# Kernel optimization log

Hardware: AMD Instinct MI355X
Metric: run time of the kernel (lower is better)

## Reference

```python
import jax, jax.numpy as jnp
import numpy as np

K = 3          # kernel_size
STRIDE = 1
ITERS = 3      # num_iterations


def squash(t, axis=-1):
    sn = jnp.sum(t * t, axis=axis, keepdims=True)
    return (sn / (1.0 + sn)) * t / jnp.sqrt(sn)


def setup_inputs() -> dict:
    key = jax.random.key(0)
    k1, k2 = jax.random.split(key)
    B, Nin, H, Cin = 8, 32, 14, 8
    C, Cout = 32, 16
    R = Nin * K * K  # 288 route nodes
    x = jax.random.normal(k1, (B, Nin, H, H, Cin), dtype=jnp.float32)
    route_weights = jax.random.normal(k2, (C, R, Cin, Cout), dtype=jnp.float32)
    return {"x": x, "route_weights": route_weights}


def reference(x, route_weights):
    B, Nin, H, _, Cin = x.shape
    C, R, _, Cout = route_weights.shape
    w = (H - K) // STRIDE + 1

    # Extract all w*w spatial windows at once (instead of the python loop).
    rows = STRIDE * jnp.arange(w)[:, None] + jnp.arange(K)  # [w, K]
    win = x[:, :, rows]            # [B, Nin, w, K, W, Cin]
    win = win[:, :, :, :, rows]    # [B, Nin, w, K, w, K, Cin]
    # route-node order matches .view: (Nin, k, k) flattened
    win = win.transpose(0, 2, 4, 1, 3, 5, 6).reshape(B, w, w, R, Cin)

    priors = jnp.einsum('bpqri,crio->cbpqro', win, route_weights)

    # Dynamic routing (fixed small iteration count -> python loop is fine).
    logits = jnp.zeros_like(priors)
    out = None
    for i in range(ITERS):
        probs = jax.nn.softmax(logits, axis=4)  # softmax over route nodes (dim=2 in torch 5D layout)
        out = squash(jnp.sum(probs * priors, axis=4, keepdims=True))  # [C,B,w,w,1,Cout]
        if i != ITERS - 1:
            logits = logits + jnp.sum(priors * out, axis=-1, keepdims=True)

    out = out[:, :, :, :, 0, :]          # [C, B, w, w, Cout]
    return out.transpose(1, 0, 2, 3, 4)  # [B, C, w, w, Cout]
```

## Files before the change

### kernel.cpp

```cpp
#include <hip/hip_runtime.h>
#include <math.h>

namespace {
constexpr int NIN   = 32;
constexpr int H_    = 14;
constexpr int CIN   = 8;
constexpr int C_    = 32;
constexpr int COUT  = 16;
constexpr int R_    = 288;
constexpr int W_    = 12;
constexpr int NITER = 3;
constexpr int CH    = 32;
constexpr int NCH   = 9;
constexpr size_t XSUB = (size_t)NIN * H_ * H_ * CIN;
}

typedef unsigned int u32;
typedef const __attribute__((address_space(1))) u32* as1_u32p;
typedef __attribute__((address_space(3))) u32* as3_u32p;

__device__ __forceinline__ void async_copy16(const void* g, void* l) {
    __builtin_amdgcn_global_load_lds((as1_u32p)g, (as3_u32p)l, 16, 0, 0);
}
__device__ __forceinline__ float dot4(const float4 a, const float4 b) {
    return fmaf(a.x, b.x, fmaf(a.y, b.y, fmaf(a.z, b.z, a.w * b.w)));
}
__device__ __forceinline__ float dpp_add_xor1(float v) {
    int t = __builtin_amdgcn_update_dpp(0, __float_as_int(v), 0xB1, 0xF, 0xF, true);
    return v + __int_as_float(t);
}
__device__ __forceinline__ float dpp_add_xor2(float v) {
    int t = __builtin_amdgcn_update_dpp(0, __float_as_int(v), 0x4E, 0xF, 0xF, true);
    return v + __int_as_float(t);
}
__device__ __forceinline__ float dpp_add_shr4(float v) {
    int t = __builtin_amdgcn_update_dpp(0, __float_as_int(v), 0x114, 0xF, 0xF, true);
    return v + __int_as_float(t);
}
__device__ __forceinline__ float dpp_add_shr8(float v) {
    int t = __builtin_amdgcn_update_dpp(0, __float_as_int(v), 0x118, 0xF, 0xF, true);
    return v + __int_as_float(t);
}
template <int CTRL>
__device__ __forceinline__ float dpp_bc(float v) {
    return __int_as_float(
        __builtin_amdgcn_update_dpp(0, __float_as_int(v), CTRL, 0xF, 0xF, true));
}

__global__ __launch_bounds__(256)
void caps_routeC(const float* __restrict__ x,
                 const float* __restrict__ rw,
                 float* __restrict__ out)
{
    const int tid = threadIdx.x;
    const int p  = blockIdx.x / W_;
    const int q  = blockIdx.x % W_;
    const int b0 = blockIdx.y * 4;
    const int c  = blockIdx.z;

    __shared__ float4 wbuf[2][1024];
    __shared__ float  sRed[4][2][16];
    __shared__ float  redE[4][2];
    __shared__ float  vS[4][16];

    const int og   = tid & 3;
    const int rl   = tid >> 2;
    const int cr   = rl & 31;
    const int sh   = rl >> 5;
    const int lane = tid & 63;
    const int wv   = tid >> 6;
    const int sA   = sh * 2;

    const float* xq = x + (size_t)(b0 + sA + (og >> 1)) * XSUB + (og & 1) * 4;
    const float4* rwcF4 = (const float4*)(rw + (size_t)c * R_ * CIN * COUT);

    float4 xv;
    auto xld = [&](int k) {
        const int r  = k * CH + cr;
        const int n  = r / 9, rem = r - n * 9;
        const int kh = rem / 3, kw = rem - kh * 3;
        xv = *(const float4*)(xq + ((n * H_ + (p + kh)) * H_ + (q + kw)) * CIN);
    };

    auto stage = [&](int k, int buf) {
        const float4* gchunk = rwcF4 + (size_t)k * (CH * 32);
        #pragma unroll
        for (int t = 0; t < 4; ++t) {
            const int s   = t * 256 + tid;
            const int ii  = s >> 7;
            const int wcr = (s >> 2) & 31;
            async_copy16(gchunk + (wcr * 32 + ii * 4 + (s & 3)),
                         (char*)&wbuf[buf][0] + (t * 256 + (tid & 192)) * 16);
        }
    };

    float4 acc[NCH][2];

    xld(0);
    stage(0, 0);
    #pragma unroll
    for (int k = 0; k < NCH; ++k) {
        __syncthreads();
        if (k + 1 < NCH) stage(k + 1, (k + 1) & 1);
        const float4* wb = &wbuf[k & 1][0];
        const float4 cur = xv;
        float fA[8], fB[8];
        fA[0] = dpp_bc<0x00>(cur.x); fA[1] = dpp_bc<0x00>(cur.y);
        fA[2] = dpp_bc<0x00>(cur.z); fA[3] = dpp_bc<0x00>(cur.w);
        fA[4] = dpp_bc<0x55>(cur.x); fA[5] = dpp_bc<0x55>(cur.y);
        fA[6] = dpp_bc<0x55>(cur.z); fA[7] = dpp_bc<0x55>(cur.w);
        fB[0] = dpp_bc<0xAA>(cur.x); fB[1] = dpp_bc<0xAA>(cur.y);
        fB[2] = dpp_bc<0xAA>(cur.z); fB[3] = dpp_bc<0xAA>(cur.w);
        fB[4] = dpp_bc<0xFF>(cur.x); fB[5] = dpp_bc<0xFF>(cur.y);
        fB[6] = dpp_bc<0xFF>(cur.z); fB[7] = dpp_bc<0xFF>(cur.w);
        if (k + 1 < NCH) xld(k + 1);
        float4 a0 = make_float4(0.f, 0.f, 0.f, 0.f);
        float4 a1 = make_float4(0.f, 0.f, 0.f, 0.f);
        #pragma unroll
        for (int i = 0; i < 8; ++i) {
            const float4 wv4 = wb[i * 128 + cr * 4 + og];
            a0.x = fmaf(fA[i], wv4.x, a0.x);  a1.x = fmaf(fB[i], wv4.x, a1.x);
            a0.y = fmaf(fA[i], wv4.y, a0.y);  a1.y = fmaf(fB[i], wv4.y, a1.y);
            a0.z = fmaf(fA[i], wv4.z, a0.z);  a1.z = fmaf(fB[i], wv4.z, a1.z);
            a0.w = fmaf(fA[i], wv4.w, a0.w);  a1.w = fmaf(fB[i], wv4.w, a1.w);
        }
        acc[k][0] = a0;  acc[k][1] = a1;
    }

    float lgA[NCH], lgB[NCH];
    #pragma unroll
    for (int j = 0; j < NCH; ++j) { lgA[j] = 0.f; lgB[j] = 0.f; }

    for (int it = 0; it < NITER; ++it) {
        float4 s0 = make_float4(0.f, 0.f, 0.f, 0.f);
        float4 s1 = make_float4(0.f, 0.f, 0.f, 0.f);
        float se0 = 0.f, se1 = 0.f;

        if (it == 0) {
            #pragma unroll
            for (int j = 0; j < NCH; ++j) {
                s0.x += acc[j][0].x;  s1.x += acc[j][1].x;
                s0.y += acc[j][0].y;  s1.y += acc[j][1].y;
                s0.z += acc[j][0].z;  s1.z += acc[j][1].z;
                s0.w += acc[j][0].w;  s1.w += acc[j][1].w;
            }
        } else {
            const float4 v0 = *(const float4*)&vS[sA][og * 4];
            const float4 v1 = *(const float4*)&vS[sA + 1][og * 4];
            #pragma unroll
            for (int j = 0; j < NCH; ++j) {
                float d0 = dot4(acc[j][0], v0);
                float d1 = dot4(acc[j][1], v1);
                d0 = dpp_add_xor1(d0);  d1 = dpp_add_xor1(d1);
                d0 = dpp_add_xor2(d0);  d1 = dpp_add_xor2(d1);
                lgA[j] += d0;                 lgB[j] += d1;
                const float e0 = __expf(lgA[j]);
                const float e1 = __expf(lgB[j]);
                se0 += e0;                    se1 += e1;
                s0.x = fmaf(e0, acc[j][0].x, s0.x);  s1.x = fmaf(e1, acc[j][1].x, s1.x);
                s0.y = fmaf(e0, acc[j][0].y, s0.y);  s1.y = fmaf(e1, acc[j][1].y, s1.y);
                s0.z = fmaf(e0, acc[j][0].z, s0.z);  s1.z = fmaf(e1, acc[j][1].z, s1.z);
                s0.w = fmaf(e0, acc[j][0].w, s0.w);  s1.w = fmaf(e1, acc[j][1].w, s1.w);
            }
            se0 = dpp_add_shr4(se0);  se1 = dpp_add_shr4(se1);
            se0 = dpp_add_shr8(se0);  se1 = dpp_add_shr8(se1);
            se0 += __shfl_xor(se0, 16, 64);  se1 += __shfl_xor(se1, 16, 64);
            se0 += __shfl_xor(se0, 32, 64);  se1 += __shfl_xor(se1, 32, 64);
            if (lane == 15) { redE[wv][0] = se0; redE[wv][1] = se1; }
        }

        s0.x = dpp_add_shr4(s0.x);  s1.x = dpp_add_shr4(s1.x);
        s0.y = dpp_add_shr4(s0.y);  s1.y = dpp_add_shr4(s1.y);
        s0.z = dpp_add_shr4(s0.z);  s1.z = dpp_add_shr4(s1.z);
        s0.w = dpp_add_shr4(s0.w);  s1.w = dpp_add_shr4(s1.w);
        s0.x = dpp_add_shr8(s0.x);  s1.x = dpp_add_shr8(s1.x);
        s0.y = dpp_add_shr8(s0.y);  s1.y = dpp_add_shr8(s1.y);
        s0.z = dpp_add_shr8(s0.z);  s1.z = dpp_add_shr8(s1.z);
        s0.w = dpp_add_shr8(s0.w);  s1.w = dpp_add_shr8(s1.w);
        #pragma unroll
        for (int off = 16; off <= 32; off <<= 1) {
            s0.x += __shfl_xor(s0.x, off, 64);  s1.x += __shfl_xor(s1.x, off, 64);
            s0.y += __shfl_xor(s0.y, off, 64);  s1.y += __shfl_xor(s1.y, off, 64);
            s0.z += __shfl_xor(s0.z, off, 64);  s1.z += __shfl_xor(s1.z, off, 64);
            s0.w += __shfl_xor(s0.w, off, 64);  s1.w += __shfl_xor(s1.w, off, 64);
        }
        if (lane >= 12 && lane < 16) {
            *(float4*)&sRed[wv][0][(lane & 3) * 4] = s0;
            *(float4*)&sRed[wv][1][(lane & 3) * 4] = s1;
        }
        __syncthreads();

        if (tid < 64) {
            const int sub = tid >> 4;
            const int o   = tid & 15;
            const int g   = sub >> 1;
            const int l   = sub & 1;
            const float inv = (it == 0)
                ? (1.0f / (float)R_)
                : 1.0f / (redE[g * 2][l] + redE[g * 2 + 1][l]);
            float s = (sRed[g * 2][l][o] + sRed[g * 2 + 1][l][o]) * inv;
            float sn = s * s;
            sn = dpp_add_xor1(sn);
            sn = dpp_add_xor2(sn);
            sn += __shfl_xor(sn, 4, 64);
            sn += __shfl_xor(sn, 8, 64);
            const float v = s * (sqrtf(sn) / (1.0f + sn));
            if (it == NITER - 1) {
                out[((((size_t)(b0 + sub) * C_ + c) * W_ + p) * W_ + q) * COUT + o] = v;
            } else {
                vS[sub][o] = v;
            }
        }
        if (it == NITER - 1) break;
        __syncthreads();
    }
}

extern "C" void kernel_launch(void* const* d_in, const int* in_sizes, int n_in,
                              void* d_out, int out_size, void* d_ws, size_t ws_size,
                              hipStream_t stream) {
    const float* x  = (const float*)d_in[0];
    const float* rw = (const float*)d_in[1];
    float* out = (float*)d_out;
    dim3 grid(W_ * W_, 2, C_);
    caps_routeC<<<grid, 256, 0, stream>>>(x, rw, out);
}
```

Baseline: 188.3 us.

## Split weight staging between LDS and registers; redundantly compute squash per thread

Half of each weight chunk (input channels 4-7) is now loaded straight from global memory into registers and prefetched one chunk ahead, while only the other half goes through the async LDS double buffer, halving the LDS staging footprint. The routing-iteration epilogue no longer funnels through a single wave writing vS. Every thread reads the double-buffered partial sums, computes the squash itself, and keeps v in registers, which removes one __syncthreads per iteration. The cost is more redundant global loads per thread and duplicated squash math, plus higher register pressure.

```diff
diff --git a/kernel.cpp b/kernel.cpp
--- a/kernel.cpp
+++ b/kernel.cpp
@@ -48,20 +48,19 @@
 }
 
 __global__ __launch_bounds__(256)
-void caps_routeC(const float* __restrict__ x,
+void caps_routeE(const float* __restrict__ x,
                  const float* __restrict__ rw,
                  float* __restrict__ out)
 {
+    __shared__ __align__(16) float4 wbuf[2][512];
+    __shared__ __align__(16) float  sRed[2][4][2][16];
+    __shared__ float  redE[2][4][2];
+
     const int tid = threadIdx.x;
     const int p  = blockIdx.x / W_;
     const int q  = blockIdx.x % W_;
     const int b0 = blockIdx.y * 4;
     const int c  = blockIdx.z;
-
-    __shared__ float4 wbuf[2][1024];
-    __shared__ float  sRed[4][2][16];
-    __shared__ float  redE[4][2];
-    __shared__ float  vS[4][16];
 
     const int og   = tid & 3;
     const int rl   = tid >> 2;
@@ -73,6 +72,7 @@
 
     const float* xq = x + (size_t)(b0 + sA + (og >> 1)) * XSUB + (og & 1) * 4;
     const float4* rwcF4 = (const float4*)(rw + (size_t)c * R_ * CIN * COUT);
+    const float4* wgbase = rwcF4 + cr * 32 + og;
 
     float4 xv;
     auto xld = [&](int k) {
@@ -82,10 +82,16 @@
         xv = *(const float4*)(xq + ((n * H_ + (p + kh)) * H_ + (q + kw)) * CIN);
     };
 
+    float4 gw0, gw1, gw2, gw3;
+    auto wld = [&](int k) {
+        const float4* g = wgbase + (size_t)k * 1024;
+        gw0 = g[16]; gw1 = g[20]; gw2 = g[24]; gw3 = g[28];
+    };
+
     auto stage = [&](int k, int buf) {
         const float4* gchunk = rwcF4 + (size_t)k * (CH * 32);
         #pragma unroll
-        for (int t = 0; t < 4; ++t) {
+        for (int t = 0; t < 2; ++t) {
             const int s   = t * 256 + tid;
             const int ii  = s >> 7;
             const int wcr = (s >> 2) & 31;
@@ -96,8 +102,7 @@
 
     float4 acc[NCH][2];
 
-    xld(0);
-    stage(0, 0);
+    xld(0); wld(0); stage(0, 0);
     #pragma unroll
     for (int k = 0; k < NCH; ++k) {
         __syncthreads();
@@ -114,10 +119,31 @@
         fB[4] = dpp_bc<0xFF>(cur.x); fB[5] = dpp_bc<0xFF>(cur.y);
         fB[6] = dpp_bc<0xFF>(cur.z); fB[7] = dpp_bc<0xFF>(cur.w);
         if (k + 1 < NCH) xld(k + 1);
+
         float4 a0 = make_float4(0.f, 0.f, 0.f, 0.f);
         float4 a1 = make_float4(0.f, 0.f, 0.f, 0.f);
+        {
+            const float4 g0 = gw0, g1 = gw1, g2 = gw2, g3 = gw3;
+            if (k + 1 < NCH) wld(k + 1);
+            a0.x = fmaf(fA[4], g0.x, a0.x);  a1.x = fmaf(fB[4], g0.x, a1.x);
+            a0.y = fmaf(fA[4], g0.y, a0.y);  a1.y = fmaf(fB[4], g0.y, a1.y);
+            a0.z = fmaf(fA[4], g0.z, a0.z);  a1.z = fmaf(fB[4], g0.z, a1.z);
+            a0.w = fmaf(fA[4], g0.w, a0.w);  a1.w = fmaf(fB[4], g0.w, a1.w);
+            a0.x = fmaf(fA[5], g1.x, a0.x);  a1.x = fmaf(fB[5], g1.x, a1.x);
+            a0.y = fmaf(fA[5], g1.y, a0.y);  a1.y = fmaf(fB[5], g1.y, a1.y);
+            a0.z = fmaf(fA[5], g1.z, a0.z);  a1.z = fmaf(fB[5], g1.z, a1.z);
+            a0.w = fmaf(fA[5], g1.w, a0.w);  a1.w = fmaf(fB[5], g1.w, a1.w);
+            a0.x = fmaf(fA[6], g2.x, a0.x);  a1.x = fmaf(fB[6], g2.x, a1.x);
+            a0.y = fmaf(fA[6], g2.y, a0.y);  a1.y = fmaf(fB[6], g2.y, a1.y);
+            a0.z = fmaf(fA[6], g2.z, a0.z);  a1.z = fmaf(fB[6], g2.z, a1.z);
+            a0.w = fmaf(fA[6], g2.w, a0.w);  a1.w = fmaf(fB[6], g2.w, a1.w);
+            a0.x = fmaf(fA[7], g3.x, a0.x);  a1.x = fmaf(fB[7], g3.x, a1.x);
+            a0.y = fmaf(fA[7], g3.y, a0.y);  a1.y = fmaf(fB[7], g3.y, a1.y);
+            a0.z = fmaf(fA[7], g3.z, a0.z);  a1.z = fmaf(fB[7], g3.z, a1.z);
+            a0.w = fmaf(fA[7], g3.w, a0.w);  a1.w = fmaf(fB[7], g3.w, a1.w);
+        }
         #pragma unroll
-        for (int i = 0; i < 8; ++i) {
+        for (int i = 0; i < 4; ++i) {
             const float4 wv4 = wb[i * 128 + cr * 4 + og];
             a0.x = fmaf(fA[i], wv4.x, a0.x);  a1.x = fmaf(fB[i], wv4.x, a1.x);
             a0.y = fmaf(fA[i], wv4.y, a0.y);  a1.y = fmaf(fB[i], wv4.y, a1.y);
@@ -130,6 +156,8 @@
     float lgA[NCH], lgB[NCH];
     #pragma unroll
     for (int j = 0; j < NCH; ++j) { lgA[j] = 0.f; lgB[j] = 0.f; }
+
+    float4 v0, v1;
 
     for (int it = 0; it < NITER; ++it) {
         float4 s0 = make_float4(0.f, 0.f, 0.f, 0.f);
@@ -145,8 +173,6 @@
                 s0.w += acc[j][0].w;  s1.w += acc[j][1].w;
             }
         } else {
-            const float4 v0 = *(const float4*)&vS[sA][og * 4];
-            const float4 v1 = *(const float4*)&vS[sA + 1][og * 4];
             #pragma unroll
             for (int j = 0; j < NCH; ++j) {
                 float d0 = dot4(acc[j][0], v0);
@@ -166,7 +192,6 @@
             se0 = dpp_add_shr8(se0);  se1 = dpp_add_shr8(se1);
             se0 += __shfl_xor(se0, 16, 64);  se1 += __shfl_xor(se1, 16, 64);
             se0 += __shfl_xor(se0, 32, 64);  se1 += __shfl_xor(se1, 32, 64);
-            if (lane == 15) { redE[wv][0] = se0; redE[wv][1] = se1; }
         }
 
         s0.x = dpp_add_shr4(s0.x);  s1.x = dpp_add_shr4(s1.x);
@@ -184,35 +209,49 @@
             s0.z += __shfl_xor(s0.z, off, 64);  s1.z += __shfl_xor(s1.z, off, 64);
             s0.w += __shfl_xor(s0.w, off, 64);  s1.w += __shfl_xor(s1.w, off, 64);
         }
+        const int ib = it & 1;
         if (lane >= 12 && lane < 16) {
-            *(float4*)&sRed[wv][0][(lane & 3) * 4] = s0;
-            *(float4*)&sRed[wv][1][(lane & 3) * 4] = s1;
-        }
+            *(float4*)&sRed[ib][wv][0][(lane & 3) * 4] = s0;
+            *(float4*)&sRed[ib][wv][1][(lane & 3) * 4] = s1;
+        }
+        if (it && lane == 15) { redE[ib][wv][0] = se0; redE[ib][wv][1] = se1; }
         __syncthreads();
 
-        if (tid < 64) {
-            const int sub = tid >> 4;
-            const int o   = tid & 15;
-            const int g   = sub >> 1;
-            const int l   = sub & 1;
-            const float inv = (it == 0)
-                ? (1.0f / (float)R_)
-                : 1.0f / (redE[g * 2][l] + redE[g * 2 + 1][l]);
-            float s = (sRed[g * 2][l][o] + sRed[g * 2 + 1][l][o]) * inv;
-            float sn = s * s;
-            sn = dpp_add_xor1(sn);
-            sn = dpp_add_xor2(sn);
-            sn += __shfl_xor(sn, 4, 64);
-            sn += __shfl_xor(sn, 8, 64);
-            const float v = s * (sqrtf(sn) / (1.0f + sn));
-            if (it == NITER - 1) {
-                out[((((size_t)(b0 + sub) * C_ + c) * W_ + p) * W_ + q) * COUT + o] = v;
-            } else {
-                vS[sub][o] = v;
+        const float4 pA0 = *(const float4*)&sRed[ib][sA][0][og * 4];
+        const float4 pB0 = *(const float4*)&sRed[ib][sA + 1][0][og * 4];
+        const float4 pA1 = *(const float4*)&sRed[ib][sA][1][og * 4];
+        const float4 pB1 = *(const float4*)&sRed[ib][sA + 1][1][og * 4];
+        float inv0, inv1;
+        if (it == 0) {
+            inv0 = inv1 = 1.0f / (float)R_;
+        } else {
+            inv0 = 1.0f / (redE[ib][sA][0] + redE[ib][sA + 1][0]);
+            inv1 = 1.0f / (redE[ib][sA][1] + redE[ib][sA + 1][1]);
+        }
+        float4 ss0, ss1;
+        ss0.x = (pA0.x + pB0.x) * inv0;  ss1.x = (pA1.x + pB1.x) * inv1;
+        ss0.y = (pA0.y + pB0.y) * inv0;  ss1.y = (pA1.y + pB1.y) * inv1;
+        ss0.z = (pA0.z + pB0.z) * inv0;  ss1.z = (pA1.z + pB1.z) * inv1;
+        ss0.w = (pA0.w + pB0.w) * inv0;  ss1.w = (pA1.w + pB1.w) * inv1;
+        float sn0 = dot4(ss0, ss0);
+        float sn1 = dot4(ss1, ss1);
+        sn0 = dpp_add_xor1(sn0);  sn1 = dpp_add_xor1(sn1);
+        sn0 = dpp_add_xor2(sn0);  sn1 = dpp_add_xor2(sn1);
+        const float c0 = sqrtf(sn0) / (1.0f + sn0);
+        const float c1 = sqrtf(sn1) / (1.0f + sn1);
+        v0.x = ss0.x * c0;  v1.x = ss1.x * c1;
+        v0.y = ss0.y * c0;  v1.y = ss1.y * c1;
+        v0.z = ss0.z * c0;  v1.z = ss1.z * c1;
+        v0.w = ss0.w * c0;  v1.w = ss1.w * c1;
+
+        if (it == NITER - 1) {
+            if (cr < 2) {
+                const float4 vv = cr ? v1 : v0;
+                *(float4*)&out[((((size_t)(b0 + sA + cr) * C_ + c) * W_ + p) * W_ + q)
+                               * COUT + og * 4] = vv;
             }
-        }
-        if (it == NITER - 1) break;
-        __syncthreads();
+            break;
+        }
     }
 }
 
@@ -223,5 +262,5 @@
     const float* rw = (const float*)d_in[1];
     float* out = (float*)d_out;
     dim3 grid(W_ * W_, 2, C_);
-    caps_routeC<<<grid, 256, 0, stream>>>(x, rw, out);
-}
+    caps_routeE<<<grid, 256, 0, stream>>>(x, rw, out);
+}
```

Measured after the change: 194.1 us. +3.0%, slower.

## Make routing kernel persistent with cross-tile prefetch of weights and inputs

Applied to the files above, without the earlier changes.

Replaces the 9216-block grid with 1024 persistent blocks that each process 9 tiles. While the last chunk of the current tile is being computed, the block issues the async LDS copy of the next tile's first weight chunk and its first x load. The aim is to cut block launch and prologue cost and to hide each tile's initial load latency. The cost is a fixed grid that may leave some CUs unevenly loaded, plus extra registers for the next tile's state.

```diff
diff --git a/kernel.cpp b/kernel.cpp
--- a/kernel.cpp
+++ b/kernel.cpp
@@ -12,6 +12,8 @@
 constexpr int NITER = 3;
 constexpr int CH    = 32;
 constexpr int NCH   = 9;
+constexpr int NTILE = 9;
+constexpr int NBLK  = 1024;
 constexpr size_t XSUB = (size_t)NIN * H_ * H_ * CIN;
 }
 
@@ -48,21 +50,16 @@
 }
 
 __global__ __launch_bounds__(256)
-void caps_routeC(const float* __restrict__ x,
+void caps_routeF(const float* __restrict__ x,
                  const float* __restrict__ rw,
                  float* __restrict__ out)
 {
-    const int tid = threadIdx.x;
-    const int p  = blockIdx.x / W_;
-    const int q  = blockIdx.x % W_;
-    const int b0 = blockIdx.y * 4;
-    const int c  = blockIdx.z;
-
     __shared__ float4 wbuf[2][1024];
     __shared__ float  sRed[4][2][16];
     __shared__ float  redE[4][2];
     __shared__ float  vS[4][16];
 
+    const int tid = threadIdx.x;
     const int og   = tid & 3;
     const int rl   = tid >> 2;
     const int cr   = rl & 31;
@@ -71,19 +68,31 @@
     const int wv   = tid >> 6;
     const int sA   = sh * 2;
 
-    const float* xq = x + (size_t)(b0 + sA + (og >> 1)) * XSUB + (og & 1) * 4;
-    const float4* rwcF4 = (const float4*)(rw + (size_t)c * R_ * CIN * COUT);
+    const size_t xlaneoff = (size_t)(sA + (og >> 1)) * XSUB + (og & 1) * 4;
+
+    const float*  xqC; const float4* rwcC; int pC, qC, b0C, cC;
+    const float*  xqN; const float4* rwcN; int pN, qN, b0N, cN;
+
+    auto mk = [&](int tile, const float*& xq_, const float4*& rwc_,
+                  int& p_, int& q_, int& b0_, int& c_) {
+        const int pq = tile % 144;
+        p_  = pq / W_;  q_ = pq % W_;
+        b0_ = ((tile / 144) & 1) * 4;
+        c_  = tile / 288;
+        xq_  = x + (size_t)b0_ * XSUB + xlaneoff;
+        rwc_ = (const float4*)(rw + (size_t)c_ * R_ * CIN * COUT);
+    };
 
     float4 xv;
-    auto xld = [&](int k) {
+    auto xld = [&](const float* xq_, int p_, int q_, int k) {
         const int r  = k * CH + cr;
         const int n  = r / 9, rem = r - n * 9;
         const int kh = rem / 3, kw = rem - kh * 3;
-        xv = *(const float4*)(xq + ((n * H_ + (p + kh)) * H_ + (q + kw)) * CIN);
+        xv = *(const float4*)(xq_ + ((n * H_ + (p_ + kh)) * H_ + (q_ + kw)) * CIN);
     };
 
-    auto stage = [&](int k, int buf) {
-        const float4* gchunk = rwcF4 + (size_t)k * (CH * 32);
+    auto stage = [&](const float4* rwc_, int k, int buf) {
+        const float4* gchunk = rwc_ + (size_t)k * (CH * 32);
         #pragma unroll
         for (int t = 0; t < 4; ++t) {
             const int s   = t * 256 + tid;
@@ -94,125 +103,143 @@
         }
     };
 
+    const int blk = blockIdx.x;
+    mk(blk, xqC, rwcC, pC, qC, b0C, cC);
+    xld(xqC, pC, qC, 0);
+    stage(rwcC, 0, 0);
+    int gbuf = 0;
+
     float4 acc[NCH][2];
 
-    xld(0);
-    stage(0, 0);
-    #pragma unroll
-    for (int k = 0; k < NCH; ++k) {
-        __syncthreads();
-        if (k + 1 < NCH) stage(k + 1, (k + 1) & 1);
-        const float4* wb = &wbuf[k & 1][0];
-        const float4 cur = xv;
-        float fA[8], fB[8];
-        fA[0] = dpp_bc<0x00>(cur.x); fA[1] = dpp_bc<0x00>(cur.y);
-        fA[2] = dpp_bc<0x00>(cur.z); fA[3] = dpp_bc<0x00>(cur.w);
-        fA[4] = dpp_bc<0x55>(cur.x); fA[5] = dpp_bc<0x55>(cur.y);
-        fA[6] = dpp_bc<0x55>(cur.z); fA[7] = dpp_bc<0x55>(cur.w);
-        fB[0] = dpp_bc<0xAA>(cur.x); fB[1] = dpp_bc<0xAA>(cur.y);
-        fB[2] = dpp_bc<0xAA>(cur.z); fB[3] = dpp_bc<0xAA>(cur.w);
-        fB[4] = dpp_bc<0xFF>(cur.x); fB[5] = dpp_bc<0xFF>(cur.y);
-        fB[6] = dpp_bc<0xFF>(cur.z); fB[7] = dpp_bc<0xFF>(cur.w);
-        if (k + 1 < NCH) xld(k + 1);
-        float4 a0 = make_float4(0.f, 0.f, 0.f, 0.f);
-        float4 a1 = make_float4(0.f, 0.f, 0.f, 0.f);
+    for (int t = 0; t < NTILE; ++t) {
+        const bool hasNext = (t + 1 < NTILE);
+
         #pragma unroll
-        for (int i = 0; i < 8; ++i) {
-            const float4 wv4 = wb[i * 128 + cr * 4 + og];
-            a0.x = fmaf(fA[i], wv4.x, a0.x);  a1.x = fmaf(fB[i], wv4.x, a1.x);
-            a0.y = fmaf(fA[i], wv4.y, a0.y);  a1.y = fmaf(fB[i], wv4.y, a1.y);
-            a0.z = fmaf(fA[i], wv4.z, a0.z);  a1.z = fmaf(fB[i], wv4.z, a1.z);
-            a0.w = fmaf(fA[i], wv4.w, a0.w);  a1.w = fmaf(fB[i], wv4.w, a1.w);
+        for (int k = 0; k < NCH; ++k) {
+            __syncthreads();
+            if (k + 1 < NCH) {
+                stage(rwcC, k + 1, gbuf ^ 1);
+            } else if (hasNext) {
+                mk(blk + NBLK * (t + 1), xqN, rwcN, pN, qN, b0N, cN);
+                stage(rwcN, 0, gbuf ^ 1);
+            }
+            const float4* wb = &wbuf[gbuf][0];
+            const float4 cur = xv;
+            float fA[8], fB[8];
+            fA[0] = dpp_bc<0x00>(cur.x); fA[1] = dpp_bc<0x00>(cur.y);
+            fA[2] = dpp_bc<0x00>(cur.z); fA[3] = dpp_bc<0x00>(cur.w);
+            fA[4] = dpp_bc<0x55>(cur.x); fA[5] = dpp_bc<0x55>(cur.y);
+            fA[6] = dpp_bc<0x55>(cur.z); fA[7] = dpp_bc<0x55>(cur.w);
+            fB[0] = dpp_bc<0xAA>(cur.x); fB[1] = dpp_bc<0xAA>(cur.y);
+            fB[2] = dpp_bc<0xAA>(cur.z); fB[3] = dpp_bc<0xAA>(cur.w);
+            fB[4] = dpp_bc<0xFF>(cur.x); fB[5] = dpp_bc<0xFF>(cur.y);
+            fB[6] = dpp_bc<0xFF>(cur.z); fB[7] = dpp_bc<0xFF>(cur.w);
+            if (k + 1 < NCH) xld(xqC, pC, qC, k + 1);
+            else if (hasNext) xld(xqN, pN, qN, 0);
+            float4 a0 = make_float4(0.f, 0.f, 0.f, 0.f);
+            float4 a1 = make_float4(0.f, 0.f, 0.f, 0.f);
+            #pragma unroll
+            for (int i = 0; i < 8; ++i) {
+                const float4 wv4 = wb[i * 128 + cr * 4 + og];
+                a0.x = fmaf(fA[i], wv4.x, a0.x);  a1.x = fmaf(fB[i], wv4.x, a1.x);
+                a0.y = fmaf(fA[i], wv4.y, a0.y);  a1.y = fmaf(fB[i], wv4.y, a1.y);
+                a0.z = fmaf(fA[i], wv4.z, a0.z);  a1.z = fmaf(fB[i], wv4.z, a1.z);
+                a0.w = fmaf(fA[i], wv4.w, a0.w);  a1.w = fmaf(fB[i], wv4.w, a1.w);
+            }
+            acc[k][0] = a0;  acc[k][1] = a1;
+            gbuf ^= 1;
         }
-        acc[k][0] = a0;  acc[k][1] = a1;
-    }
-
-    float lgA[NCH], lgB[NCH];
-    #pragma unroll
-    for (int j = 0; j < NCH; ++j) { lgA[j] = 0.f; lgB[j] = 0.f; }
-
-    for (int it = 0; it < NITER; ++it) {
-        float4 s0 = make_float4(0.f, 0.f, 0.f, 0.f);
-        float4 s1 = make_float4(0.f, 0.f, 0.f, 0.f);
-        float se0 = 0.f, se1 = 0.f;
-
-        if (it == 0) {
+
+        float lgA[NCH], lgB[NCH];
+        #pragma unroll
+        for (int j = 0; j < NCH; ++j) { lgA[j] = 0.f; lgB[j] = 0.f; }
+
+        for (int it = 0; it < NITER; ++it) {
+            float4 s0 = make_float4(0.f, 0.f, 0.f, 0.f);
+            float4 s1 = make_float4(0.f, 0.f, 0.f, 0.f);
+            float se0 = 0.f, se1 = 0.f;
+
+            if (it == 0) {
+                #pragma unroll
+                for (int j = 0; j < NCH; ++j) {
+                    s0.x += acc[j][0].x;  s1.x += acc[j][1].x;
+                    s0.y += acc[j][0].y;  s1.y += acc[j][1].y;
+                    s0.z += acc[j][0].z;  s1.z += acc[j][1].z;
+                    s0.w += acc[j][0].w;  s1.w += acc[j][1].w;
+                }
+            } else {
+                const float4 v0 = *(const float4*)&vS[sA][og * 4];
+                const float4 v1 = *(const float4*)&vS[sA + 1][og * 4];
+                #pragma unroll
+                for (int j = 0; j < NCH; ++j) {
+                    float d0 = dot4(acc[j][0], v0);
+                    float d1 = dot4(acc[j][1], v1);
+                    d0 = dpp_add_xor1(d0);  d1 = dpp_add_xor1(d1);
+                    d0 = dpp_add_xor2(d0);  d1 = dpp_add_xor2(d1);
+                    lgA[j] += d0;                 lgB[j] += d1;
+                    const float e0 = __expf(lgA[j]);
+                    const float e1 = __expf(lgB[j]);
+                    se0 += e0;                    se1 += e1;
+                    s0.x = fmaf(e0, acc[j][0].x, s0.x);  s1.x = fmaf(e1, acc[j][1].x, s1.x);
+                    s0.y = fmaf(e0, acc[j][0].y, s0.y);  s1.y = fmaf(e1, acc[j][1].y, s1.y);
+                    s0.z = fmaf(e0, acc[j][0].z, s0.z);  s1.z = fmaf(e1, acc[j][1].z, s1.z);
+                    s0.w = fmaf(e0, acc[j][0].w, s0.w);  s1.w = fmaf(e1, acc[j][1].w, s1.w);
+                }
+                se0 = dpp_add_shr4(se0);  se1 = dpp_add_shr4(se1);
+                se0 = dpp_add_shr8(se0);  se1 = dpp_add_shr8(se1);
+                se0 += __shfl_xor(se0, 16, 64);  se1 += __shfl_xor(se1, 16, 64);
+                se0 += __shfl_xor(se0, 32, 64);  se1 += __shfl_xor(se1, 32, 64);
+                if (lane == 15) { redE[wv][0] = se0; redE[wv][1] = se1; }
+            }
+
+            s0.x = dpp_add_shr4(s0.x);  s1.x = dpp_add_shr4(s1.x);
+            s0.y = dpp_add_shr4(s0.y);  s1.y = dpp_add_shr4(s1.y);
+            s0.z = dpp_add_shr4(s0.z);  s1.z = dpp_add_shr4(s1.z);
+            s0.w = dpp_add_shr4(s0.w);  s1.w = dpp_add_shr4(s1.w);
+            s0.x = dpp_add_shr8(s0.x);  s1.x = dpp_add_shr8(s1.x);
+            s0.y = dpp_add_shr8(s0.y);  s1.y = dpp_add_shr8(s1.y);
+            s0.z = dpp_add_shr8(s0.z);  s1.z = dpp_add_shr8(s1.z);
+            s0.w = dpp_add_shr8(s0.w);  s1.w = dpp_add_shr8(s1.w);
             #pragma unroll
-            for (int j = 0; j < NCH; ++j) {
-                s0.x += acc[j][0].x;  s1.x += acc[j][1].x;
-                s0.y += acc[j][0].y;  s1.y += acc[j][1].y;
-                s0.z += acc[j][0].z;  s1.z += acc[j][1].z;
-                s0.w += acc[j][0].w;  s1.w += acc[j][1].w;
-            }
-        } else {
-            const float4 v0 = *(const float4*)&vS[sA][og * 4];
-            const float4 v1 = *(const float4*)&vS[sA + 1][og * 4];
-            #pragma unroll
-            for (int j = 0; j < NCH; ++j) {
-                float d0 = dot4(acc[j][0], v0);
-                float d1 = dot4(acc[j][1], v1);
-                d0 = dpp_add_xor1(d0);  d1 = dpp_add_xor1(d1);
-                d0 = dpp_add_xor2(d0);  d1 = dpp_add_xor2(d1);
-                lgA[j] += d0;                 lgB[j] += d1;
-                const float e0 = __expf(lgA[j]);
-                const float e1 = __expf(lgB[j]);
-                se0 += e0;                    se1 += e1;
-                s0.x = fmaf(e0, acc[j][0].x, s0.x);  s1.x = fmaf(e1, acc[j][1].x, s1.x);
-                s0.y = fmaf(e0, acc[j][0].y, s0.y);  s1.y = fmaf(e1, acc[j][1].y, s1.y);
-                s0.z = fmaf(e0, acc[j][0].z, s0.z);  s1.z = fmaf(e1, acc[j][1].z, s1.z);
-                s0.w = fmaf(e0, acc[j][0].w, s0.w);  s1.w = fmaf(e1, acc[j][1].w, s1.w);
-            }
-            se0 = dpp_add_shr4(se0);  se1 = dpp_add_shr4(se1);
-            se0 = dpp_add_shr8(se0);  se1 = dpp_add_shr8(se1);
-            se0 += __shfl_xor(se0, 16, 64);  se1 += __shfl_xor(se1, 16, 64);
-            se0 += __shfl_xor(se0, 32, 64);  se1 += __shfl_xor(se1, 32, 64);
-            if (lane == 15) { redE[wv][0] = se0; redE[wv][1] = se1; }
+            for (int off = 16; off <= 32; off <<= 1) {
+                s0.x += __shfl_xor(s0.x, off, 64);  s1.x += __shfl_xor(s1.x, off, 64);
+                s0.y += __shfl_xor(s0.y, off, 64);  s1.y += __shfl_xor(s1.y, off, 64);
+                s0.z += __shfl_xor(s0.z, off, 64);  s1.z += __shfl_xor(s1.z, off, 64);
+                s0.w += __shfl_xor(s0.w, off, 64);  s1.w += __shfl_xor(s1.w, off, 64);
+            }
+            if (lane >= 12 && lane < 16) {
+                *(float4*)&sRed[wv][0][(lane & 3) * 4] = s0;
+                *(float4*)&sRed[wv][1][(lane & 3) * 4] = s1;
+            }
+            __syncthreads();
+
+            if (tid < 64) {
+                const int sub = tid >> 4;
+                const int o   = tid & 15;
+                const int g   = sub >> 1;
+                const int l   = sub & 1;
+                const float inv = (it == 0)
+                    ? (1.0f / (float)R_)
+                    : 1.0f / (redE[g * 2][l] + redE[g * 2 + 1][l]);
+                float s = (sRed[g * 2][l][o] + sRed[g * 2 + 1][l][o]) * inv;
+                float sn = s * s;
+                sn = dpp_add_xor1(sn);
+                sn = dpp_add_xor2(sn);
+                sn += __shfl_xor(sn, 4, 64);
+                sn += __shfl_xor(sn, 8, 64);
+                const float v = s * (sqrtf(sn) / (1.0f + sn));
+                if (it == NITER - 1) {
+                    out[((((size_t)(b0C + sub) * C_ + cC) * W_ + pC) * W_ + qC)
+                        * COUT + o] = v;
+                } else {
+                    vS[sub][o] = v;
+                }
+            }
+            if (it == NITER - 1) break;
+            __syncthreads();
         }
 
-        s0.x = dpp_add_shr4(s0.x);  s1.x = dpp_add_shr4(s1.x);
-        s0.y = dpp_add_shr4(s0.y);  s1.y = dpp_add_shr4(s1.y);
-        s0.z = dpp_add_shr4(s0.z);  s1.z = dpp_add_shr4(s1.z);
-        s0.w = dpp_add_shr4(s0.w);  s1.w = dpp_add_shr4(s1.w);
-        s0.x = dpp_add_shr8(s0.x);  s1.x = dpp_add_shr8(s1.x);
-        s0.y = dpp_add_shr8(s0.y);  s1.y = dpp_add_shr8(s1.y);
-        s0.z = dpp_add_shr8(s0.z);  s1.z = dpp_add_shr8(s1.z);
-        s0.w = dpp_add_shr8(s0.w);  s1.w = dpp_add_shr8(s1.w);
-        #pragma unroll
-        for (int off = 16; off <= 32; off <<= 1) {
-            s0.x += __shfl_xor(s0.x, off, 64);  s1.x += __shfl_xor(s1.x, off, 64);
-            s0.y += __shfl_xor(s0.y, off, 64);  s1.y += __shfl_xor(s1.y, off, 64);
-            s0.z += __shfl_xor(s0.z, off, 64);  s1.z += __shfl_xor(s1.z, off, 64);
-            s0.w += __shfl_xor(s0.w, off, 64);  s1.w += __shfl_xor(s1.w, off, 64);
-        }
-        if (lane >= 12 && lane < 16) {
-            *(float4*)&sRed[wv][0][(lane & 3) * 4] = s0;
-            *(float4*)&sRed[wv][1][(lane & 3) * 4] = s1;
-        }
-        __syncthreads();
-
-        if (tid < 64) {
-            const int sub = tid >> 4;
-            const int o   = tid & 15;
-            const int g   = sub >> 1;
-            const int l   = sub & 1;
-            const float inv = (it == 0)
-                ? (1.0f / (float)R_)
-                : 1.0f / (redE[g * 2][l] + redE[g * 2 + 1][l]);
-            float s = (sRed[g * 2][l][o] + sRed[g * 2 + 1][l][o]) * inv;
-            float sn = s * s;
-            sn = dpp_add_xor1(sn);
-            sn = dpp_add_xor2(sn);
-            sn += __shfl_xor(sn, 4, 64);
-            sn += __shfl_xor(sn, 8, 64);
-            const float v = s * (sqrtf(sn) / (1.0f + sn));
-            if (it == NITER - 1) {
-                out[((((size_t)(b0 + sub) * C_ + c) * W_ + p) * W_ + q) * COUT + o] = v;
-            } else {
-                vS[sub][o] = v;
-            }
-        }
-        if (it == NITER - 1) break;
-        __syncthreads();
+        xqC = xqN; rwcC = rwcN; pC = pN; qC = qN; b0C = b0N; cC = cN;
     }
 }
 
@@ -222,6 +249,5 @@
     const float* x  = (const float*)d_in[0];
     const float* rw = (const float*)d_in[1];
     float* out = (float*)d_out;
-    dim3 grid(W_ * W_, 2, C_);
-    caps_routeC<<<grid, 256, 0, stream>>>(x, rw, out);
-}
+    caps_routeF<<<dim3(NBLK), 256, 0, stream>>>(x, rw, out);
+}
```

Result: slower. 353.1 us (+87.5%).
